# Performance work log

Measured on AMD Instinct MI355X. Metric: run time of the kernel, lower is better.

The kernel has to match this reference:

```python
import jax, jax.numpy as jnp
import numpy as np


def setup_inputs() -> dict:
    key = jax.random.key(0)
    ks = jax.random.split(key, 9)
    n_cells, n_pix = 512, 160 * 160
    n_bins_filter, max_c = 100, 20
    n_frames, n_bins_total, n_init = 300, 1500, 100
    # scale filters so the generator signal stays O(1) (avoids sigmoid saturation)
    return {
        "initial_spikes": jax.random.uniform(ks[0], (n_cells, n_init), jnp.float32),
        "input_frames": jax.random.uniform(ks[1], (n_frames, n_pix), jnp.float32),
        "spat_filters": jax.random.normal(ks[2], (n_cells, n_pix), jnp.float32) * 0.005,
        "feedback_filters": jax.random.normal(ks[3], (n_cells, n_bins_filter), jnp.float32) * 0.05,
        "coupling_filters": jax.random.normal(ks[4], (n_cells, max_c, n_bins_filter), jnp.float32) * 0.02,
        "bias": jax.random.normal(ks[5], (n_cells, 1), jnp.float32) * 0.1,
        "forward_weights": jax.random.uniform(ks[6], (n_bins_total, 2), jnp.float32),
        "coupled_sel": jax.random.randint(ks[7], (n_cells, max_c), 0, n_cells),
        "forward_sel": jnp.sort(jax.random.randint(ks[8], (n_bins_total, 2), 0, n_frames), axis=1),
    }


def reference(initial_spikes, input_frames, spat_filters, feedback_filters,
              coupling_filters, bias, forward_weights, coupled_sel, forward_sel):
    n_cells, n_bins_filter = feedback_filters.shape
    n_init = initial_spikes.shape[1]

    # stimulus drive: spatial filtering then temporal upsampling frames -> bins
    spat = input_frames @ spat_filters.T                       # (F, C)
    ups = jnp.einsum('tkc,tk->ct', spat[forward_sel], forward_weights)  # (C, T)
    stim = ups + bias                                          # (C, T)

    window0 = initial_spikes[:, n_init - n_bins_filter:]       # (C, B)
    xs = stim[:, n_init - 1:-1].T                              # (T - n_init, C), stim[:, i-1]

    def step(window, stim_t):
        fb = jnp.einsum('cb,cb->c', window, feedback_filters)
        gathered = window[coupled_sel]                         # (C, M, B)
        cp = jnp.einsum('cmb,cmb->c', gathered, coupling_filters)
        gensig = stim_t + cp + fb
        spikes = jax.nn.sigmoid(gensig)                        # spike_generation_callable
        window = jnp.concatenate([window[:, 1:], spikes[:, None]], axis=1)
        return window, spikes

    _, ys = jax.lax.scan(step, window0, xs)                    # ys: (T - n_init, C)
    return jnp.concatenate([initial_spikes, ys.T], axis=1)     # (C, T)
```

## Files before the change

kernel.cpp:

```cpp
#include <hip/hip_runtime.h>
#include <hip/hip_bf16.h>

#define N_CELLS  512
#define N_PIX    25600
#define NBF      100
#define MAXC     20
#define N_FRAMES 300
#define NBT      1500
#define N_INIT   100
#define T_STEPS  (NBT - N_INIT)

#define RING   104
#define RSTR   105
#define NWG    64
#define CPW    (N_CELLS / NWG)
#define SCAN_THREADS (CPW * 64)
#define XDEPTH 8

#define GT 64
#define GC 64
#define GK 64
#define KSPLIT 8
#define KCH (N_PIX / KSPLIT)

__global__ __launch_bounds__(256) void gemm_partial_k(
        const float* __restrict__ A,
        const float* __restrict__ B,
        float* __restrict__ part)
{
    __shared__ float As[GK][GT + 4];
    __shared__ float Bs[GK][GC + 4];
    const int kb = blockIdx.x, tb = blockIdx.y, cb = blockIdx.z;
    const int tid = threadIdx.x;
    const int tx = tid & 15, ty = tid >> 4;
    const int t0 = tb * GT, c0 = cb * GC, k0 = kb * KCH;

    float acc[4][4];
    #pragma unroll
    for (int i = 0; i < 4; ++i)
        #pragma unroll
        for (int j = 0; j < 4; ++j) acc[i][j] = 0.f;

    for (int kc = 0; kc < KCH; kc += GK) {
        #pragma unroll
        for (int p = 0; p < 4; ++p) {
            const int r  = (tid >> 4) + p * 16;
            const int kk = (tid & 15) * 4;
            float4 av = make_float4(0.f, 0.f, 0.f, 0.f);
            if (t0 + r < N_FRAMES)
                av = *(const float4*)&A[(size_t)(t0 + r) * N_PIX + k0 + kc + kk];
            As[kk + 0][r] = av.x; As[kk + 1][r] = av.y;
            As[kk + 2][r] = av.z; As[kk + 3][r] = av.w;
            const float4 bv = *(const float4*)&B[(size_t)(c0 + r) * N_PIX + k0 + kc + kk];
            Bs[kk + 0][r] = bv.x; Bs[kk + 1][r] = bv.y;
            Bs[kk + 2][r] = bv.z; Bs[kk + 3][r] = bv.w;
        }
        __syncthreads();
        #pragma unroll
        for (int kk = 0; kk < GK; ++kk) {
            const float4 a4 = *(const float4*)&As[kk][ty * 4];
            const float4 b4 = *(const float4*)&Bs[kk][tx * 4];
            const float aa[4] = {a4.x, a4.y, a4.z, a4.w};
            const float bb[4] = {b4.x, b4.y, b4.z, b4.w};
            #pragma unroll
            for (int ii = 0; ii < 4; ++ii)
                #pragma unroll
                for (int jj = 0; jj < 4; ++jj)
                    acc[ii][jj] = fmaf(aa[ii], bb[jj], acc[ii][jj]);
        }
        __syncthreads();
    }
    #pragma unroll
    for (int ii = 0; ii < 4; ++ii) {
        const int t = t0 + ty * 4 + ii;
        if (t < N_FRAMES) {
            #pragma unroll
            for (int jj = 0; jj < 4; ++jj)
                part[(size_t)kb * (N_FRAMES * N_CELLS) + (size_t)t * N_CELLS + c0 + tx * 4 + jj] = acc[ii][jj];
        }
    }
}

__global__ void reduce_part_k(const float* __restrict__ part, float* __restrict__ spat) {
    int i = blockIdx.x * 256 + threadIdx.x;
    if (i < N_FRAMES * N_CELLS) {
        float s = 0.f;
        #pragma unroll
        for (int kb = 0; kb < KSPLIT; ++kb) s += part[(size_t)kb * (N_FRAMES * N_CELLS) + i];
        spat[i] = s;
    }
}

__global__ void stim_k(const float* __restrict__ spat, const float* __restrict__ bias,
                       const float* __restrict__ fw, const int* __restrict__ fs,
                       float* __restrict__ stimb) {
    int i = blockIdx.x * 256 + threadIdx.x;
    if (i < NBT * N_CELLS) {
        const int t = i >> 9, c = i & (N_CELLS - 1);
        const int t2 = t * 2;
        float v = bias[c];
        v = fmaf(fw[t2],     spat[(size_t)fs[t2]     * N_CELLS + c], v);
        v = fmaf(fw[t2 + 1], spat[(size_t)fs[t2 + 1] * N_CELLS + c], v);
        stimb[i] = v;
    }
}

__global__ void copy_init_k(const float* __restrict__ ini, float* __restrict__ out) {
    int i = blockIdx.x * 256 + threadIdx.x;
    if (i < N_CELLS * N_INIT) {
        const int c = i / N_INIT;
        const int j = i - c * N_INIT;
        out[(size_t)c * NBT + j] = ini[i];
    }
}

__device__ __forceinline__ int wrap_slot(int t) {
    int s = t % RING;
    return (s < 0) ? s + RING : s;
}

__global__ __launch_bounds__(SCAN_THREADS) void scan_k(
        const float* __restrict__ stimb,
        const float* __restrict__ cf,
        const float* __restrict__ ff,
        const int*   __restrict__ sel,
        const float* __restrict__ ini,
        unsigned long long* __restrict__ X64,
        float* __restrict__ out)
{
    __shared__ __hip_bfloat16 win[N_CELLS][RSTR];
    __shared__ float newspike[N_CELLS];
    __shared__ int   lag1src[CPW][32];
    __shared__ float lag1coef[CPW][32];

    const int wg   = blockIdx.x;
    const int tid  = threadIdx.x;
    const int wave = tid >> 6;
    const int lane = tid & 63;
    const int cell = wg * CPW + wave;

    int   srcm[MAXC + 1];
    float c1v[MAXC + 1], c2v[MAXC + 1];
    #pragma unroll
    for (int m = 0; m <= MAXC; ++m) {
        const int s = (m < MAXC) ? sel[cell * MAXC + m] : cell;
        const float* f = (m < MAXC) ? (cf + (size_t)(cell * MAXC + m) * NBF)
                                    : (ff + (size_t)cell * NBF);
        srcm[m] = s;
        c1v[m]  = f[98 - lane];
        c2v[m]  = (lane <= 34) ? f[34 - lane] : 0.f;
        if (lane == m) {
            lag1src[wave][m]  = s;
            lag1coef[wave][m] = f[NBF - 1];
        }
    }

    {
        __hip_bfloat16* wf = &win[0][0];
        for (int i = tid; i < N_CELLS * RSTR; i += SCAN_THREADS) wf[i] = __float2bfloat16(0.f);
        __syncthreads();
        for (int i = tid; i < N_CELLS * N_INIT; i += SCAN_THREADS) {
            const int c = i / N_INIT;
            const int b = i - c * N_INIT;
            win[c][wrap_slot(b - N_INIT)] = __float2bfloat16(ini[i]);
        }
    }
    __syncthreads();

    int slotp1 = wrap_slot(-2 - lane);
    int slotp2 = wrap_slot(-66 - lane);
    int slotw  = RING - 1;

    const float ini_last = ini[tid * N_INIT + (N_INIT - 1)];

    float stim_next = 0.f;
    if (lane == 0) stim_next = stimb[(size_t)(N_INIT - 1) * N_CELLS + cell];

    float partial;
    {
        float p = 0.f;
        #pragma unroll
        for (int m = 0; m <= MAXC; ++m) {
            const float w1 = __bfloat162float(win[srcm[m]][slotp1]);
            const float w2 = __bfloat162float(win[srcm[m]][slotp2]);
            p = fmaf(w1, c1v[m], p);
            p = fmaf(w2, c2v[m], p);
        }
        #pragma unroll
        for (int off = 32; off > 0; off >>= 1) p += __shfl_xor(p, off, 64);
        partial = p;
    }

    for (int i = 0; i < T_STEPS; ++i) {
        float val;
        if (i > 0) {
            const unsigned long long* wp = &X64[(size_t)((i - 1) & (XDEPTH - 1)) * N_CELLS + tid];
            unsigned long long w;
            do {
                w = __hip_atomic_load(wp, __ATOMIC_RELAXED, __HIP_MEMORY_SCOPE_AGENT);
            } while ((unsigned)(w >> 32) != (unsigned)i);
            val = __uint_as_float((unsigned)w);
        } else {
            val = ini_last;
        }

        newspike[tid] = val;
        win[tid][slotw] = __float2bfloat16(val);
        __syncthreads();

        float term = 0.f;
        if (lane <= MAXC) {
            term = newspike[lag1src[wave][lane]] * lag1coef[wave][lane];
        }
        #pragma unroll
        for (int off = 32; off > 0; off >>= 1) term += __shfl_xor(term, off, 64);

        if (lane == 0) {
            const float g = stim_next + partial + term;
            const float sp = 1.f / (1.f + __expf(-g));
            const unsigned long long pw =
                ((unsigned long long)(unsigned)(i + 1) << 32) |
                (unsigned long long)__float_as_uint(sp);
            __hip_atomic_store(&X64[(size_t)(i & (XDEPTH - 1)) * N_CELLS + cell], pw,
                               __ATOMIC_RELAXED, __HIP_MEMORY_SCOPE_AGENT);
            out[(size_t)cell * NBT + N_INIT + i] = sp;
        }

        slotw  = (slotw  + 1 == RING) ? 0 : slotw  + 1;
        slotp1 = (slotp1 + 1 == RING) ? 0 : slotp1 + 1;
        slotp2 = (slotp2 + 1 == RING) ? 0 : slotp2 + 1;

        if (lane == 0 && i + 1 < T_STEPS)
            stim_next = stimb[(size_t)(N_INIT + i) * N_CELLS + cell];

        float p = 0.f;
        #pragma unroll
        for (int m = 0; m <= MAXC; ++m) {
            const float w1 = __bfloat162float(win[srcm[m]][slotp1]);
            const float w2 = __bfloat162float(win[srcm[m]][slotp2]);
            p = fmaf(w1, c1v[m], p);
            p = fmaf(w2, c2v[m], p);
        }
        #pragma unroll
        for (int off = 32; off > 0; off >>= 1) p += __shfl_xor(p, off, 64);
        partial = p;
    }
}

extern "C" void kernel_launch(void* const* d_in, const int* in_sizes, int n_in,
                              void* d_out, int out_size, void* d_ws, size_t ws_size,
                              hipStream_t stream) {
    const float* ini    = (const float*)d_in[0];
    const float* frames = (const float*)d_in[1];
    const float* sfil   = (const float*)d_in[2];
    const float* ff     = (const float*)d_in[3];
    const float* cf     = (const float*)d_in[4];
    const float* bias   = (const float*)d_in[5];
    const float* fw     = (const float*)d_in[6];
    const int*   sel    = (const int*)d_in[7];
    const int*   fs     = (const int*)d_in[8];
    float* out = (float*)d_out;
    float* ws  = (float*)d_ws;

    float* spat  = ws;
    float* stimb = ws + 153600;
    unsigned long long* X64 = (unsigned long long*)(ws + 153600 + 768000);
    float* part  = ws + 153600;

    hipLaunchKernelGGL(gemm_partial_k,
                       dim3(KSPLIT, (N_FRAMES + GT - 1) / GT, N_CELLS / GC), dim3(256), 0, stream,
                       frames, sfil, part);
    hipLaunchKernelGGL(reduce_part_k, dim3((N_FRAMES * N_CELLS + 255) / 256), dim3(256), 0, stream, part, spat);
    hipLaunchKernelGGL(stim_k, dim3((NBT * N_CELLS + 255) / 256), dim3(256), 0, stream, spat, bias, fw, fs, stimb);
    hipMemsetAsync(X64, 0, (size_t)XDEPTH * N_CELLS * sizeof(unsigned long long), stream);
    hipLaunchKernelGGL(copy_init_k, dim3((N_CELLS * N_INIT + 255) / 256), dim3(256), 0, stream, ini, out);
    hipLaunchKernelGGL(scan_k, dim3(NWG), dim3(SCAN_THREADS), 0, stream,
                       stimb, cf, ff, sel, ini, X64, out);
}
```

Measured before the change: 2.236 ms.

## Decouple cross-workgroup spike exchange with 3-step lag and packed bf16 flags

The scan now computes the three most recent lags (1–3) for each cell's 21 sources directly in registers. Each source lane polls only its own source's flag word. The full shared-memory window is filled from global memory with a 3-step delay, so the block-wide barrier no longer waits on the newest step's remote values. The exchange word shrinks from 64-bit to 32-bit, packing a 16-bit step tag with a bf16 spike. This is meant to take the global poll off the per-step critical path. In exchange, the lag-1..3 spikes are rounded to bf16, and the 16-bit tag can still tell steps apart across the 1400 steps because the ring is only 8 deep.

Measured after the change: 2.890 ms. +29.3%, slower.

```diff
diff --git a/kernel.cpp b/kernel.cpp
--- a/kernel.cpp
+++ b/kernel.cpp
@@ -1,5 +1,6 @@
 #include <hip/hip_runtime.h>
 #include <hip/hip_bf16.h>
+#include <stdint.h>
 
 #define N_CELLS  512
 #define N_PIX    25600
@@ -125,19 +126,29 @@
         const float* __restrict__ ff,
         const int*   __restrict__ sel,
         const float* __restrict__ ini,
-        unsigned long long* __restrict__ X64,
+        uint32_t* __restrict__ X32,
         float* __restrict__ out)
 {
     __shared__ __hip_bfloat16 win[N_CELLS][RSTR];
-    __shared__ float newspike[N_CELLS];
-    __shared__ int   lag1src[CPW][32];
-    __shared__ float lag1coef[CPW][32];
-
-    const int wg   = blockIdx.x;
+
     const int tid  = threadIdx.x;
     const int wave = tid >> 6;
     const int lane = tid & 63;
-    const int cell = wg * CPW + wave;
+    const int cell = blockIdx.x * CPW + wave;
+
+    int psrc = 0;
+    float pc1 = 0.f, pc2 = 0.f, pc3 = 0.f;
+    float y0 = 0.f, y1 = 0.f, y2 = 0.f;
+    if (lane <= MAXC) {
+        const int s = (lane < MAXC) ? sel[cell * MAXC + lane] : cell;
+        const float* f = (lane < MAXC) ? (cf + (size_t)(cell * MAXC + lane) * NBF)
+                                       : (ff + (size_t)cell * NBF);
+        psrc = s;
+        pc1 = f[99]; pc2 = f[98]; pc3 = f[97];
+        y0 = ini[s * N_INIT + 99];
+        y1 = ini[s * N_INIT + 98];
+        y2 = ini[s * N_INIT + 97];
+    }
 
     int   srcm[MAXC + 1];
     float c1v[MAXC + 1], c2v[MAXC + 1];
@@ -147,12 +158,8 @@
         const float* f = (m < MAXC) ? (cf + (size_t)(cell * MAXC + m) * NBF)
                                     : (ff + (size_t)cell * NBF);
         srcm[m] = s;
-        c1v[m]  = f[98 - lane];
-        c2v[m]  = (lane <= 34) ? f[34 - lane] : 0.f;
-        if (lane == m) {
-            lag1src[wave][m]  = s;
-            lag1coef[wave][m] = f[NBF - 1];
-        }
+        c1v[m]  = f[96 - lane];
+        c2v[m]  = (lane <= 32) ? f[32 - lane] : 0.f;
     }
 
     {
@@ -167,24 +174,19 @@
     }
     __syncthreads();
 
-    int slotp1 = wrap_slot(-2 - lane);
-    int slotp2 = wrap_slot(-66 - lane);
-    int slotw  = RING - 1;
-
-    const float ini_last = ini[tid * N_INIT + (N_INIT - 1)];
-
-    float stim_next = 0.f;
-    if (lane == 0) stim_next = stimb[(size_t)(N_INIT - 1) * N_CELLS + cell];
+    int sp1 = wrap_slot(-4 - lane);
+    int sp2 = wrap_slot(-68 - lane);
+    int ws  = 0;
+
+    float stim_cur = (lane == 0) ? stimb[(size_t)(N_INIT - 1) * N_CELLS + cell] : 0.f;
 
     float partial;
     {
         float p = 0.f;
         #pragma unroll
         for (int m = 0; m <= MAXC; ++m) {
-            const float w1 = __bfloat162float(win[srcm[m]][slotp1]);
-            const float w2 = __bfloat162float(win[srcm[m]][slotp2]);
-            p = fmaf(w1, c1v[m], p);
-            p = fmaf(w2, c2v[m], p);
+            p = fmaf(__bfloat162float(win[srcm[m]][sp1]), c1v[m], p);
+            p = fmaf(__bfloat162float(win[srcm[m]][sp2]), c2v[m], p);
         }
         #pragma unroll
         for (int off = 32; off > 0; off >>= 1) p += __shfl_xor(p, off, 64);
@@ -192,58 +194,62 @@
     }
 
     for (int i = 0; i < T_STEPS; ++i) {
-        float val;
         if (i > 0) {
-            const unsigned long long* wp = &X64[(size_t)((i - 1) & (XDEPTH - 1)) * N_CELLS + tid];
-            unsigned long long w;
+            y2 = y1; y1 = y0;
+            if (lane <= MAXC) {
+                const uint32_t* wp = &X32[(size_t)((i - 1) & (XDEPTH - 1)) * N_CELLS + psrc];
+                uint32_t w;
+                do {
+                    w = __hip_atomic_load(wp, __ATOMIC_RELAXED, __HIP_MEMORY_SCOPE_AGENT);
+                } while ((w >> 16) != (uint32_t)i);
+                y0 = __uint_as_float((w & 0xffffu) << 16);
+            }
+        }
+        float term = y0 * pc1;
+        term = fmaf(y1, pc2, term);
+        term = fmaf(y2, pc3, term);
+        #pragma unroll
+        for (int off = 16; off > 0; off >>= 1) term += __shfl_xor(term, off, 32);
+
+        if (lane == 0) {
+            const float g = stim_cur + partial + term;
+            const float s = 1.f / (1.f + __expf(-g));
+            __hip_bfloat16 hb = __float2bfloat16(s);
+            const uint32_t us = (uint32_t)*reinterpret_cast<unsigned short*>(&hb);
+            const uint32_t pw = ((uint32_t)(i + 1) << 16) | us;
+            __hip_atomic_store(&X32[(size_t)(i & (XDEPTH - 1)) * N_CELLS + cell], pw,
+                               __ATOMIC_RELAXED, __HIP_MEMORY_SCOPE_AGENT);
+            out[(size_t)cell * NBT + N_INIT + i] = s;
+        }
+
+        const int j = i - 3;
+        if (j >= 0) {
+            const uint32_t* ip = &X32[(size_t)(j & (XDEPTH - 1)) * N_CELLS + tid];
+            uint32_t w;
             do {
-                w = __hip_atomic_load(wp, __ATOMIC_RELAXED, __HIP_MEMORY_SCOPE_AGENT);
-            } while ((unsigned)(w >> 32) != (unsigned)i);
-            val = __uint_as_float((unsigned)w);
-        } else {
-            val = ini_last;
-        }
-
-        newspike[tid] = val;
-        win[tid][slotw] = __float2bfloat16(val);
-        __syncthreads();
-
-        float term = 0.f;
-        if (lane <= MAXC) {
-            term = newspike[lag1src[wave][lane]] * lag1coef[wave][lane];
-        }
-        #pragma unroll
-        for (int off = 32; off > 0; off >>= 1) term += __shfl_xor(term, off, 64);
-
-        if (lane == 0) {
-            const float g = stim_next + partial + term;
-            const float sp = 1.f / (1.f + __expf(-g));
-            const unsigned long long pw =
-                ((unsigned long long)(unsigned)(i + 1) << 32) |
-                (unsigned long long)__float_as_uint(sp);
-            __hip_atomic_store(&X64[(size_t)(i & (XDEPTH - 1)) * N_CELLS + cell], pw,
-                               __ATOMIC_RELAXED, __HIP_MEMORY_SCOPE_AGENT);
-            out[(size_t)cell * NBT + N_INIT + i] = sp;
-        }
-
-        slotw  = (slotw  + 1 == RING) ? 0 : slotw  + 1;
-        slotp1 = (slotp1 + 1 == RING) ? 0 : slotp1 + 1;
-        slotp2 = (slotp2 + 1 == RING) ? 0 : slotp2 + 1;
-
-        if (lane == 0 && i + 1 < T_STEPS)
-            stim_next = stimb[(size_t)(N_INIT + i) * N_CELLS + cell];
-
+                w = __hip_atomic_load(ip, __ATOMIC_RELAXED, __HIP_MEMORY_SCOPE_AGENT);
+            } while ((w >> 16) != (uint32_t)(j + 1));
+            unsigned short us = (unsigned short)(w & 0xffffu);
+            win[tid][ws] = *reinterpret_cast<__hip_bfloat16*>(&us);
+            ws = (ws + 1 == RING) ? 0 : ws + 1;
+        }
+        float stim_next = 0.f;
+        if (lane == 0) stim_next = stimb[(size_t)(N_INIT + i) * N_CELLS + cell];
+
+        __syncthreads();
+
+        sp1 = (sp1 + 1 == RING) ? 0 : sp1 + 1;
+        sp2 = (sp2 + 1 == RING) ? 0 : sp2 + 1;
         float p = 0.f;
         #pragma unroll
         for (int m = 0; m <= MAXC; ++m) {
-            const float w1 = __bfloat162float(win[srcm[m]][slotp1]);
-            const float w2 = __bfloat162float(win[srcm[m]][slotp2]);
-            p = fmaf(w1, c1v[m], p);
-            p = fmaf(w2, c2v[m], p);
+            p = fmaf(__bfloat162float(win[srcm[m]][sp1]), c1v[m], p);
+            p = fmaf(__bfloat162float(win[srcm[m]][sp2]), c2v[m], p);
         }
         #pragma unroll
         for (int off = 32; off > 0; off >>= 1) p += __shfl_xor(p, off, 64);
         partial = p;
+        stim_cur = stim_next;
     }
 }
 
@@ -264,7 +270,7 @@
 
     float* spat  = ws;
     float* stimb = ws + 153600;
-    unsigned long long* X64 = (unsigned long long*)(ws + 153600 + 768000);
+    uint32_t* X32 = (uint32_t*)(ws + 153600 + 768000);
     float* part  = ws + 153600;
 
     hipLaunchKernelGGL(gemm_partial_k,
@@ -272,8 +278,8 @@
                        frames, sfil, part);
     hipLaunchKernelGGL(reduce_part_k, dim3((N_FRAMES * N_CELLS + 255) / 256), dim3(256), 0, stream, part, spat);
     hipLaunchKernelGGL(stim_k, dim3((NBT * N_CELLS + 255) / 256), dim3(256), 0, stream, spat, bias, fw, fs, stimb);
-    hipMemsetAsync(X64, 0, (size_t)XDEPTH * N_CELLS * sizeof(unsigned long long), stream);
+    hipMemsetAsync(X32, 0, (size_t)XDEPTH * N_CELLS * sizeof(uint32_t), stream);
     hipLaunchKernelGGL(copy_init_k, dim3((N_CELLS * N_INIT + 255) / 256), dim3(256), 0, stream, ini, out);
     hipLaunchKernelGGL(scan_k, dim3(NWG), dim3(SCAN_THREADS), 0, stream,
-                       stimb, cf, ff, sel, ini, X64, out);
-}
+                       stimb, cf, ff, sel, ini, X32, out);
+}
```
